# Kernel optimization log

Measured on AMD Instinct MI355X. Metric: run time of the kernel, lower is better.

Reference implementation:

```python
import jax, jax.numpy as jnp
import numpy as np

D_MODEL, D_STATE, EXPAND = 256, 16, 2
D_INNER = EXPAND * D_MODEL
DT_RANK = (D_MODEL + 15) // 16
BATCH, SEQLEN = 4, 4096


def silu(x):
    return x * jax.nn.sigmoid(x)


def setup_inputs() -> dict:
    key = jax.random.key(0)
    ks = jax.random.split(key, 10)
    h = jax.random.normal(ks[0], (BATCH, SEQLEN, D_MODEL), dtype=jnp.float32)
    Wi_f = jax.random.normal(ks[1], (2 * D_INNER, D_MODEL), dtype=jnp.float32) / np.sqrt(D_MODEL)
    Wi_b = jax.random.normal(ks[2], (2 * D_INNER, D_MODEL), dtype=jnp.float32) / np.sqrt(D_MODEL)
    Wx_f = jax.random.normal(ks[3], (DT_RANK + 2 * D_STATE, D_INNER), dtype=jnp.float32) / np.sqrt(D_INNER)
    Wx_b = jax.random.normal(ks[4], (DT_RANK + 2 * D_STATE, D_INNER), dtype=jnp.float32) / np.sqrt(D_INNER)
    dt_std = DT_RANK ** -0.5
    Wdt_f = jax.random.uniform(ks[5], (D_INNER, DT_RANK), dtype=jnp.float32, minval=-dt_std, maxval=dt_std)
    Wdt_b = jax.random.uniform(ks[6], (D_INNER, DT_RANK), dtype=jnp.float32, minval=-dt_std, maxval=dt_std)
    # dt bias = inverse-softplus of dt sampled log-uniform in [1e-3, 1e-1]
    dt = jnp.exp(jax.random.uniform(ks[7], (D_INNER,), dtype=jnp.float32) * (np.log(0.1) - np.log(0.001)) + np.log(0.001))
    dt = jnp.clip(dt, 1e-4, None)
    inv_dt = dt + jnp.log(-jnp.expm1(-dt))
    bdt_f = inv_dt
    bdt_b = inv_dt
    A_log = jnp.log(jnp.broadcast_to(jnp.arange(1, D_STATE + 1, dtype=jnp.float32), (D_INNER, D_STATE)))
    A_log_f = A_log
    A_log_b = A_log
    D_f = jnp.ones((D_INNER,), dtype=jnp.float32)
    D_b = jnp.ones((D_INNER,), dtype=jnp.float32)
    Wo = jax.random.normal(ks[8], (D_MODEL, 2 * D_INNER), dtype=jnp.float32) / np.sqrt(2 * D_INNER)
    return {"hidden_states": h, "Wi_f": Wi_f, "Wi_b": Wi_b, "Wx_f": Wx_f, "Wx_b": Wx_b,
            "Wdt_f": Wdt_f, "Wdt_b": Wdt_b, "bdt_f": bdt_f, "bdt_b": bdt_b,
            "A_log_f": A_log_f, "A_log_b": A_log_b, "D_f": D_f, "D_b": D_b, "Wo": Wo}


def mamba_dir(h, Wi, Wx, Wdt, bdt, A_log, Dp, reverse):
    b, l, _ = h.shape
    di, r = Wdt.shape
    n = A_log.shape[1]
    xz = h @ Wi.T                      # [b,l,2*di]
    if reverse:
        xz = xz[:, ::-1]
    x, z = xz[..., :di], xz[..., di:]
    u = silu(x)                        # selective_scan input u
    x_dbl = u @ Wx.T                   # [b,l,r+2n]
    delta = jax.nn.softplus(x_dbl[..., :r] @ Wdt.T + bdt)   # [b,l,di]
    Bm = x_dbl[..., r:r + n]           # [b,l,n]
    Cm = x_dbl[..., r + n:r + 2 * n]   # [b,l,n]
    A = -jnp.exp(A_log)                # [di,n]

    def step(s, inp):
        u_t, d_t, B_t, C_t = inp       # [b,di],[b,di],[b,n],[b,n]
        dA = jnp.exp(d_t[..., None] * A)                         # [b,di,n]
        s = dA * s + (d_t * u_t)[..., None] * B_t[:, None, :]    # [b,di,n]
        y_t = jnp.einsum('bdn,bn->bd', s, C_t)
        return s, y_t

    s0 = jnp.zeros((b, di, n), dtype=u.dtype)
    xs = (jnp.swapaxes(u, 0, 1), jnp.swapaxes(delta, 0, 1),
          jnp.swapaxes(Bm, 0, 1), jnp.swapaxes(Cm, 0, 1))
    _, ys = jax.lax.scan(step, s0, xs)
    y = jnp.swapaxes(ys, 0, 1) + u * Dp          # skip term D*u
    y = y * silu(z)                              # gated output
    if reverse:
        y = y[:, ::-1]
    return y


def reference(hidden_states, Wi_f, Wi_b, Wx_f, Wx_b, Wdt_f, Wdt_b, bdt_f, bdt_b, A_log_f, A_log_b, D_f, D_b, Wo):
    y_f = mamba_dir(hidden_states, Wi_f, Wx_f, Wdt_f, bdt_f, A_log_f, D_f, False)
    y_b = mamba_dir(hidden_states, Wi_b, Wx_b, Wdt_b, bdt_b, A_log_b, D_b, True)
    y = jnp.concatenate([y_f, y_b], axis=-1)     # [b,l,2*di]
    return y @ Wo.T                              # [b,l,d_model]
```

## Files before the change

### kernel.cpp

```cpp
#include <hip/hip_runtime.h>
#include <hip/hip_bf16.h>
#include <cstddef>
#include <cstdint>

#define D_MODELc 256
#define D_STATEc 16
#define D_INNERc 512
#define DT_RANKc 16
#define BATCHc   4
#define SEQLENc  4096
#define NCHUNK   128
#define CHUNK    32

typedef unsigned short u16;
typedef __attribute__((ext_vector_type(8))) short bf16x8;
typedef __attribute__((ext_vector_type(4))) float f32x4;
typedef float __attribute__((ext_vector_type(4))) f4v;

__device__ __forceinline__ float siluf(float v) { return v / (1.f + __expf(-v)); }

__device__ __forceinline__ u16 bf16_rne(float f) {
    uint32_t u = __float_as_uint(f);
    u += 0x7fffu + ((u >> 16) & 1u);
    return (u16)(u >> 16);
}
__device__ __forceinline__ float bf16_to_f(u16 h) {
    return __uint_as_float(((uint32_t)h) << 16);
}
__device__ __forceinline__ uint32_t pack_hl(float f) {
    u16 hh = bf16_rne(f);
    u16 ll = bf16_rne(f - bf16_to_f(hh));
    return ((uint32_t)hh << 16) | ll;
}
__device__ __forceinline__ float unpack_add(uint32_t v) {
    return __uint_as_float(v & 0xFFFF0000u) + __uint_as_float(v << 16);
}
__device__ __forceinline__ void unpack_frag(const uint32_t* q, bf16x8& fh, bf16x8& fl) {
    union { bf16x8 v; uint32_t w[4]; } H, L;
    #pragma unroll
    for (int i = 0; i < 4; i++) {
        uint32_t a = q[2 * i], b = q[2 * i + 1];
        H.w[i] = (a >> 16) | (b & 0xFFFF0000u);
        L.w[i] = (a & 0xFFFFu) | (b << 16);
    }
    fh = H.v; fl = L.v;
}
__device__ __forceinline__ float softplusf(float x) {
    return fmaxf(x, 0.f) + __logf(1.f + __expf(-fabsf(x)));
}
__device__ __forceinline__ float dot16_tree(const f4v x[4], const float* w, float bias) {
    float t0 = fmaf(x[0][1], w[1],  x[0][0] * w[0]);
    float t1 = fmaf(x[0][3], w[3],  x[0][2] * w[2]);
    float t2 = fmaf(x[1][1], w[5],  x[1][0] * w[4]);
    float t3 = fmaf(x[1][3], w[7],  x[1][2] * w[6]);
    float t4 = fmaf(x[2][1], w[9],  x[2][0] * w[8]);
    float t5 = fmaf(x[2][3], w[11], x[2][2] * w[10]);
    float t6 = fmaf(x[3][1], w[13], x[3][0] * w[12]);
    float t7 = fmaf(x[3][3], w[15], x[3][2] * w[14]);
    return bias + (((t0 + t1) + (t2 + t3)) + ((t4 + t5) + (t6 + t7)));
}
__device__ __forceinline__ void qladder(float q, float* qd) {
    float q2 = q * q;
    float q4 = q2 * q2;
    float q8 = q4 * q4;
    qd[0] = q;        qd[1] = q2;       qd[2] = q2 * q;     qd[3] = q4;
    qd[4] = q4 * q;   qd[5] = q4 * q2;  qd[6] = q4 * qd[2]; qd[7] = q8;
    qd[8] = q8 * q;   qd[9] = q8 * q2;  qd[10] = q8 * qd[2]; qd[11] = q8 * q4;
    qd[12] = q8 * qd[4]; qd[13] = q8 * qd[5]; qd[14] = q8 * qd[6]; qd[15] = q8 * q8;
}

#define GLL16(g, l) __builtin_amdgcn_global_load_lds( \
    (const __attribute__((address_space(1))) uint32_t*)(g), \
    (__attribute__((address_space(3))) uint32_t*)(l), 16, 0, 0)

__global__ __launch_bounds__(256) void split5_kernel(
        const float* __restrict__ s0, const float* __restrict__ s1,
        const float* __restrict__ s2, const float* __restrict__ s3,
        const float* __restrict__ s4,
        u16* __restrict__ h0, u16* __restrict__ l0,
        u16* __restrict__ h1, u16* __restrict__ l1,
        u16* __restrict__ h2, u16* __restrict__ l2,
        u16* __restrict__ h3, u16* __restrict__ l3,
        u16* __restrict__ h4, u16* __restrict__ l4,
        int n4w, int n4x) {
    const int which = blockIdx.y;
    const float* in; u16* hi; u16* lo; int n4;
    if      (which == 0) { in = s0; hi = h0; lo = l0; n4 = n4w; }
    else if (which == 1) { in = s1; hi = h1; lo = l1; n4 = n4w; }
    else if (which == 2) { in = s2; hi = h2; lo = l2; n4 = n4w; }
    else if (which == 3) { in = s3; hi = h3; lo = l3; n4 = n4x; }
    else                 { in = s4; hi = h4; lo = l4; n4 = n4x; }
    for (int i = blockIdx.x * 256 + threadIdx.x; i < n4; i += gridDim.x * 256) {
        float4 v = ((const float4*)in)[i];
        u16 a0 = bf16_rne(v.x), a1 = bf16_rne(v.y), a2 = bf16_rne(v.z), a3 = bf16_rne(v.w);
        ushort4 hv; hv.x = a0; hv.y = a1; hv.z = a2; hv.w = a3;
        ushort4 lv;
        lv.x = bf16_rne(v.x - bf16_to_f(a0));
        lv.y = bf16_rne(v.y - bf16_to_f(a1));
        lv.z = bf16_rne(v.z - bf16_to_f(a2));
        lv.w = bf16_rne(v.w - bf16_to_f(a3));
        ((ushort4*)hi)[i] = hv;
        ((ushort4*)lo)[i] = lv;
    }
}

__global__ __launch_bounds__(256) void split_kernel(const float* __restrict__ in,
                                                    u16* __restrict__ hi,
                                                    u16* __restrict__ lo, int n4) {
    int i = blockIdx.x * 256 + threadIdx.x;
    const int stride = gridDim.x * 256;
    for (; i < n4; i += stride) {
        float4 v = ((const float4*)in)[i];
        u16 a0 = bf16_rne(v.x), a1 = bf16_rne(v.y), a2 = bf16_rne(v.z), a3 = bf16_rne(v.w);
        ushort4 hv; hv.x = a0; hv.y = a1; hv.z = a2; hv.w = a3;
        ushort4 lv;
        lv.x = bf16_rne(v.x - bf16_to_f(a0));
        lv.y = bf16_rne(v.y - bf16_to_f(a1));
        lv.z = bf16_rne(v.z - bf16_to_f(a2));
        lv.w = bf16_rne(v.w - bf16_to_f(a3));
        ((ushort4*)hi)[i] = hv;
        ((ushort4*)lo)[i] = lv;
    }
}

template<int EPI, int NBL2, int AINT>
__global__ __launch_bounds__(256) void gemm_mfma(
        const u16* __restrict__ Ah, const u16* __restrict__ Al, int lda,
        const u16* __restrict__ Bh, const u16* __restrict__ Bl, int ldb,
        float* __restrict__ out0,
        uint32_t* __restrict__ uhl,
        int M, int N, int K) {
    __shared__ char lds[2][32768];
    const int t    = threadIdx.x;
    const int lane = t & 63;
    const int wid  = t >> 6;
    const int wrow = wid >> 1, wcol = wid & 1;

    const int id  = blockIdx.x;
    const int xcd = id & 7;
    const int j   = id >> 3;
    const int nb  = j & ((1 << NBL2) - 1);
    const int mg  = j >> NBL2;
    const int m0  = (mg * 8 + xcd) * 128;
    const int n0  = nb * 128;

    const int lr  = lane & 15;
    const int kgl = lane >> 4;

    f32x4 acc[4][4] = {};

    const char* gp[8];
    if (AINT == 0) {
        #pragma unroll
        for (int i = 0; i < 8; i++) {
            int c    = i * 256 + t;
            int tile = c >> 9;
            int kg   = (c >> 7) & 3;
            int row  = c & 127;
            const u16* bsrc = (tile == 0) ? Ah : (tile == 1) ? Al : (tile == 2) ? Bh : Bl;
            int r0 = (tile < 2) ? m0 : n0;
            int ld = (tile < 2) ? lda : ldb;
            gp[i] = (const char*)(bsrc + (size_t)(r0 + row) * ld + kg * 8);
        }
    } else {
        #pragma unroll
        for (int i = 0; i < 4; i++) {
            int c    = i * 256 + t;
            int kg   = c >> 8;
            int row  = (c >> 1) & 127;
            int half = c & 1;
            gp[i] = (const char*)((const uint32_t*)Ah + (size_t)(m0 + row) * lda + kg * 8 + half * 4);
        }
        #pragma unroll
        for (int i = 4; i < 8; i++) {
            int cb   = (i - 4) * 256 + t;
            int tile = cb >> 9;
            int kg   = (cb >> 7) & 3;
            int row  = cb & 127;
            const u16* bsrc = tile ? Bl : Bh;
            gp[i] = (const char*)(bsrc + (size_t)(n0 + row) * ldb + kg * 8);
        }
    }
    const int ldst_t = t << 4;

    auto stage = [&](int buf) {
        #pragma unroll
        for (int i = 0; i < 8; i++) {
            GLL16(gp[i], ((char*)lds) + buf * 32768 + i * 4096 + ldst_t);
            gp[i] += (AINT == 1 && i < 4) ? 128 : 64;
        }
    };

    const int NT = K >> 5;
    stage(0);
    __syncthreads();

    for (int kt = 0; kt < NT; ++kt) {
        const int buf = kt & 1;
        if (kt + 1 < NT) stage(buf ^ 1);

        bf16x8 afh[4], afl[4];
        if (AINT == 0) {
            const u16* lb = (const u16*)lds[buf];
            #pragma unroll
            for (int mi = 0; mi < 4; mi++) {
                int row = wrow * 64 + mi * 16 + lr;
                afh[mi] = *(const bf16x8*)(lb + 0 * 4096 + kgl * 1024 + row * 8);
                afl[mi] = *(const bf16x8*)(lb + 1 * 4096 + kgl * 1024 + row * 8);
            }
        } else {
            const uint32_t* la = (const uint32_t*)lds[buf];
            #pragma unroll
            for (int mi = 0; mi < 4; mi++) {
                int row = wrow * 64 + mi * 16 + lr;
                unpack_frag(la + kgl * 1024 + row * 8, afh[mi], afl[mi]);
            }
        }
        const u16* lbB = (const u16*)(lds[buf] + 16384);
        #pragma unroll
        for (int ni = 0; ni < 4; ni++) {
            int row = wcol * 64 + ni * 16 + lr;
            bf16x8 bfh = *(const bf16x8*)(lbB + 0 * 4096 + kgl * 1024 + row * 8);
            bf16x8 bfl = *(const bf16x8*)(lbB + 1 * 4096 + kgl * 1024 + row * 8);
            #pragma unroll
            for (int mi = 0; mi < 4; mi++) {
                acc[mi][ni] = __builtin_amdgcn_mfma_f32_16x16x32_bf16(afh[mi], bfh, acc[mi][ni], 0, 0, 0);
                acc[mi][ni] = __builtin_amdgcn_mfma_f32_16x16x32_bf16(afh[mi], bfl, acc[mi][ni], 0, 0, 0);
                acc[mi][ni] = __builtin_amdgcn_mfma_f32_16x16x32_bf16(afl[mi], bfh, acc[mi][ni], 0, 0, 0);
            }
        }
        __syncthreads();
    }

    #pragma unroll
    for (int mi = 0; mi < 4; mi++) {
        #pragma unroll
        for (int ni = 0; ni < 4; ni++) {
            #pragma unroll
            for (int r = 0; r < 4; r++) {
                int m = m0 + wrow * 64 + mi * 16 + kgl * 4 + r;
                int n = n0 + wcol * 64 + ni * 16 + lr;
                float v = acc[mi][ni][r];
                if (EPI == 0) {
                    __builtin_nontemporal_store(v, &out0[(size_t)m * N + n]);
                } else {
                    float s = siluf(v);
                    int dirn = n >> 10;
                    int nn   = n & 1023;
                    size_t dof = (size_t)dirn * (size_t)M * 512;
                    if (nn < 512) {
                        uhl[dof + (size_t)m * 512 + nn] = pack_hl(s);
                    } else {
                        out0[dof + (size_t)m * 512 + (nn - 512)] = s;
                    }
                }
            }
        }
    }
}

__global__ __launch_bounds__(256) void xdbl_mfma(
        const uint32_t* __restrict__ Uhl,
        const u16* __restrict__ WxH, const u16* __restrict__ WxL,
        float* __restrict__ out) {
    __shared__ uint32_t lds[4][64][8];
    const int t    = threadIdx.x;
    const int lane = t & 63;
    const int wid  = t >> 6;
    const int m0   = blockIdx.x * 64;
    const int dir  = blockIdx.y;
    const int Mp   = gridDim.x * 64;
    const int lr   = lane & 15;
    const int kgl  = lane >> 4;

    const size_t dofU = (size_t)dir * (size_t)Mp * 512;
    const size_t dofW = (size_t)dir * (size_t)48 * 512;

    const char* gp[2];
    #pragma unroll
    for (int i = 0; i < 2; i++) {
        int c    = i * 256 + t;
        int kg   = c >> 7;
        int row  = (c >> 1) & 63;
        int half = c & 1;
        gp[i] = (const char*)(Uhl + dofU + (size_t)(m0 + row) * 512 + kg * 8 + half * 4);
    }
    const int ldst_t = t << 4;

    f32x4 acc[3] = {};

    for (int k0 = 0; k0 < 512; k0 += 32) {
        #pragma unroll
        for (int i = 0; i < 2; i++) {
            GLL16(gp[i], ((char*)lds) + i * 4096 + ldst_t);
            gp[i] += 128;
        }
        __syncthreads();

        bf16x8 afh, afl;
        unpack_frag(&lds[kgl][wid * 16 + lr][0], afh, afl);
        #pragma unroll
        for (int nf = 0; nf < 3; nf++) {
            const size_t boff = dofW + (size_t)(nf * 16 + lr) * 512 + k0 + kgl * 8;
            bf16x8 bfh = *(const bf16x8*)(WxH + boff);
            bf16x8 bfl = *(const bf16x8*)(WxL + boff);
            acc[nf] = __builtin_amdgcn_mfma_f32_16x16x32_bf16(afh, bfh, acc[nf], 0, 0, 0);
            acc[nf] = __builtin_amdgcn_mfma_f32_16x16x32_bf16(afh, bfl, acc[nf], 0, 0, 0);
            acc[nf] = __builtin_amdgcn_mfma_f32_16x16x32_bf16(afl, bfh, acc[nf], 0, 0, 0);
        }
        __syncthreads();
    }

    float* o = out + (size_t)dir * (size_t)Mp * 48;
    #pragma unroll
    for (int nf = 0; nf < 3; nf++) {
        #pragma unroll
        for (int r = 0; r < 4; r++) {
            int m = m0 + wid * 16 + kgl * 4 + r;
            int n = nf * 16 + lr;
            o[(size_t)m * 48 + n] = acc[nf][r];
        }
    }
}

__global__ __launch_bounds__(256) void scan_phaseA(
        const uint32_t* __restrict__ Uhl,
        const float* __restrict__ XD,
        const float* __restrict__ Wdt_f, const float* __restrict__ Wdt_b,
        const float* __restrict__ bdt_f, const float* __restrict__ bdt_b,
        const float* __restrict__ AL_f, const float* __restrict__ AL_b,
        float* __restrict__ SDL, float* __restrict__ S) {
    const int c   = blockIdx.x;
    const int d   = blockIdx.y * 256 + threadIdx.x;
    const int z   = blockIdx.z;
    const int dir = z & 1;
    const int b   = z >> 1;
    const int PB  = gridDim.z >> 1;
    const int Mp  = PB * SEQLENc;
    const float* Wdt = dir ? Wdt_b : Wdt_f;
    const float* bdt = dir ? bdt_b : bdt_f;
    const float* AL  = dir ? AL_b  : AL_f;
    const uint32_t* UD = Uhl + (size_t)dir * Mp * 512;
    const float* XDD = XD + (size_t)dir * Mp * 48;

    float w[16], a[16], s[16];
    #pragma unroll
    for (int n = 0; n < 16; n++) {
        w[n] = Wdt[d * 16 + n];
        a[n] = -__expf(AL[d * 16 + n]);
        s[n] = 0.f;
    }
    const float a0 = a[0];
    bool pw = (a0 != 0.f);
    #pragma unroll
    for (int n = 1; n < 16; n++)
        pw = pw && (fabsf(a[n] - (float)(n + 1) * a0) <= 3e-6f * fabsf(a[n]));
    const float bb = bdt[d];
    float sdl = 0.f;

    for (int i = 0; i < CHUNK; i++) {
        int tt = c * CHUNK + i;
        int l  = dir ? (SEQLENc - 1 - tt) : tt;
        size_t row = (size_t)b * SEQLENc + l;
        float uu = unpack_add(UD[row * 512 + d]);
        const f4v* xr4 = (const f4v*)&XDD[row * 48];
        f4v xw[4] = {xr4[0], xr4[1], xr4[2], xr4[3]};
        float dl = softplusf(dot16_tree(xw, w, bb));
        sdl += dl;
        float du = dl * uu;
        if (pw) {
            float qd[16];
            qladder(__expf(a0 * dl), qd);
            #pragma unroll
            for (int g = 0; g < 4; g++) {
                f4v B4 = xr4[4 + g];
                #pragma unroll
                for (int jj = 0; jj < 4; jj++) {
                    int n = g * 4 + jj;
                    s[n] = fmaf(qd[n], s[n], du * B4[jj]);
                }
            }
        } else {
            #pragma unroll
            for (int g = 0; g < 4; g++) {
                f4v B4 = xr4[4 + g];
                #pragma unroll
                for (int jj = 0; jj < 4; jj++) {
                    int n = g * 4 + jj;
                    float dA = __expf(dl * a[n]);
                    s[n] = fmaf(dA, s[n], du * B4[jj]);
                }
            }
        }
    }
    SDL[((size_t)z * NCHUNK + c) * 512 + d] = sdl;
    size_t base = (((size_t)z * NCHUNK + c) * 16) * 512 + d;
    #pragma unroll
    for (int n = 0; n < 16; n++)
        S[base + (size_t)n * 512] = s[n];
}

__global__ __launch_bounds__(256) void scan_phaseB(const float* __restrict__ SDL,
                                                   float* __restrict__ S,
                                                   const float* __restrict__ AL_f,
                                                   const float* __restrict__ AL_b) {
    const int g   = blockIdx.x * 256 + threadIdx.x;
    const int d   = g & 511;
    const int n   = (g >> 9) & 15;
    const int z   = g >> 13;
    const int dir = z & 1;
    const float an = -__expf((dir ? AL_b : AL_f)[d * 16 + n]);
    const size_t strideS = (size_t)16 * 512;
    size_t offS = (((size_t)z * NCHUNK) * 16 + n) * 512 + d;
    size_t offD = ((size_t)z * NCHUNK) * 512 + d;
    float carry = 0.f;
    float sdl = SDL[offD], ss = S[offS];
    for (int c = 0; c < NCHUNK; c++) {
        float sdn = 0.f, sn = 0.f;
        if (c + 1 < NCHUNK) { sdn = SDL[offD + 512]; sn = S[offS + strideS]; }
        float pp = __expf(an * sdl);
        S[offS] = carry;
        carry = pp * carry + ss;
        sdl = sdn; ss = sn;
        offS += strideS; offD += 512;
    }
}

__global__ __launch_bounds__(256) void scan_phaseC(
        const uint32_t* __restrict__ Uhl,
        const float* __restrict__ XD,
        const float* __restrict__ Wdt_f, const float* __restrict__ Wdt_b,
        const float* __restrict__ bdt_f, const float* __restrict__ bdt_b,
        const float* __restrict__ AL_f, const float* __restrict__ AL_b,
        const float* __restrict__ E,
        const float* __restrict__ SZ,
        const float* __restrict__ D_f,  const float* __restrict__ D_b,
        uint32_t* __restrict__ Yhl) {
    const int c   = blockIdx.x;
    const int d   = blockIdx.y * 256 + threadIdx.x;
    const int z   = blockIdx.z;
    const int dir = z & 1;
    const int b   = z >> 1;
    const int PB  = gridDim.z >> 1;
    const int Mp  = PB * SEQLENc;
    const float* Wdt = dir ? Wdt_b : Wdt_f;
    const float* bdt = dir ? bdt_b : bdt_f;
    const float* AL  = dir ? AL_b  : AL_f;
    const uint32_t* UD = Uhl + (size_t)dir * Mp * 512;
    const float* XDD = XD + (size_t)dir * Mp * 48;
    const float* SZD = SZ + (size_t)dir * Mp * 512;

    float w[16], a[16], s[16];
    size_t base = (((size_t)z * NCHUNK + c) * 16) * 512 + d;
    #pragma unroll
    for (int n = 0; n < 16; n++) {
        w[n] = Wdt[d * 16 + n];
        a[n] = -__expf(AL[d * 16 + n]);
        s[n] = E[base + (size_t)n * 512];
    }
    const float a0 = a[0];
    bool pw = (a0 != 0.f);
    #pragma unroll
    for (int n = 1; n < 16; n++)
        pw = pw && (fabsf(a[n] - (float)(n + 1) * a0) <= 3e-6f * fabsf(a[n]));
    const float bb = bdt[d];
    const float Dd = (dir ? D_b : D_f)[d];

    for (int i = 0; i < CHUNK; i++) {
        int tt = c * CHUNK + i;
        int l  = dir ? (SEQLENc - 1 - tt) : tt;
        size_t row = (size_t)b * SEQLENc + l;
        float uu = unpack_add(UD[row * 512 + d]);
        const f4v* xr4 = (const f4v*)&XDD[row * 48];
        f4v xw[4] = {xr4[0], xr4[1], xr4[2], xr4[3]};
        float dl = softplusf(dot16_tree(xw, w, bb));
        float du = dl * uu;
        float yp0 = 0.f, yp1 = 0.f, yp2 = 0.f, yp3 = 0.f;
        if (pw) {
            float qd[16];
            qladder(__expf(a0 * dl), qd);
            #pragma unroll
            for (int g = 0; g < 4; g++) {
                f4v B4 = xr4[4 + g];
                f4v C4 = xr4[8 + g];
                float yp = 0.f;
                #pragma unroll
                for (int jj = 0; jj < 4; jj++) {
                    int n = g * 4 + jj;
                    s[n] = fmaf(qd[n], s[n], du * B4[jj]);
                    yp = fmaf(s[n], C4[jj], yp);
                }
                if (g == 0) yp0 = yp; else if (g == 1) yp1 = yp;
                else if (g == 2) yp2 = yp; else yp3 = yp;
            }
        } else {
            #pragma unroll
            for (int g = 0; g < 4; g++) {
                f4v B4 = xr4[4 + g];
                f4v C4 = xr4[8 + g];
                float yp = 0.f;
                #pragma unroll
                for (int jj = 0; jj < 4; jj++) {
                    int n = g * 4 + jj;
                    float dA = __expf(dl * a[n]);
                    s[n] = fmaf(dA, s[n], du * B4[jj]);
                    yp = fmaf(s[n], C4[jj], yp);
                }
                if (g == 0) yp0 = yp; else if (g == 1) yp1 = yp;
                else if (g == 2) yp2 = yp; else yp3 = yp;
            }
        }
        float y = (yp0 + yp1) + (yp2 + yp3);
        float sz = SZD[row * 512 + d];
        float yv = (y + uu * Dd) * sz;
        Yhl[row * 1024 + (size_t)dir * 512 + d] = pack_hl(yv);
    }
}

extern "C" void kernel_launch(void* const* d_in, const int* in_sizes, int n_in,
                              void* d_out, int out_size, void* d_ws, size_t ws_size,
                              hipStream_t stream) {
    const float* h    = (const float*)d_in[0];
    const float* Wi_f = (const float*)d_in[1];
    const float* Wi_b = (const float*)d_in[2];
    const float* Wx_f = (const float*)d_in[3];
    const float* Wx_b = (const float*)d_in[4];
    const float* Wdt_f= (const float*)d_in[5];
    const float* Wdt_b= (const float*)d_in[6];
    const float* bdt_f= (const float*)d_in[7];
    const float* bdt_b= (const float*)d_in[8];
    const float* Al_f = (const float*)d_in[9];
    const float* Al_b = (const float*)d_in[10];
    const float* D_f  = (const float*)d_in[11];
    const float* D_b  = (const float*)d_in[12];
    const float* Wo   = (const float*)d_in[13];
    float* out = (float*)d_out;

    const size_t W_ELE  = 1024 * 256;
    const size_t WX_ELE = 48 * 512;
    const size_t FB   = (size_t)SEQLENc * D_INNERc;
    const size_t FH   = (size_t)SEQLENc * D_MODELc;
    const size_t FX   = (size_t)SEQLENc * 48;
    const size_t FP   = (size_t)NCHUNK * 16 * 512;
    const size_t FD   = (size_t)NCHUNK * 512;
    const size_t FY   = (size_t)SEQLENc * 1024;

    const size_t fixed_bytes = (8 * W_ELE + 4 * WX_ELE) * sizeof(u16);
    const size_t per_b = 2 * FH * sizeof(u16)
                       + 2 * FB * sizeof(float)
                       + 2 * FB * sizeof(uint32_t)
                       + 2 * FX * sizeof(float)
                       + 2 * (FP + FD) * sizeof(float)
                       + FY * sizeof(uint32_t);
    int PB = 4;
    if (fixed_bytes + 4 * per_b + 65536 > ws_size) PB = 2;
    if (fixed_bytes + 2 * per_b + 65536 > ws_size) PB = 1;

    char* cur = (char*)d_ws;
    auto alloc = [&](size_t bytes) -> char* {
        char* p = cur; cur += (bytes + 255) & ~(size_t)255; return p;
    };
    u16* WiH = (u16*)alloc(2 * W_ELE * 2);
    u16* WiL = (u16*)alloc(2 * W_ELE * 2);
    u16* WoH = (u16*)alloc(W_ELE * 2);
    u16* WoL = (u16*)alloc(W_ELE * 2);
    u16* WxH = (u16*)alloc(2 * WX_ELE * 2);
    u16* WxL = (u16*)alloc(2 * WX_ELE * 2);
    u16*      hH  = (u16*)alloc((size_t)PB * FH * 2);
    u16*      hL  = (u16*)alloc((size_t)PB * FH * 2);
    float*    sz  = (float*)alloc((size_t)PB * 2 * FB * 4);
    uint32_t* uhl = (uint32_t*)alloc((size_t)PB * 2 * FB * 4);
    float*    xd  = (float*)alloc((size_t)PB * 2 * FX * 4);
    float*    SDL = (float*)alloc((size_t)PB * 2 * FD * 4);
    float*    S   = (float*)alloc((size_t)PB * 2 * FP * 4);
    uint32_t* yhl = (uint32_t*)alloc((size_t)PB * FY * 4);

    {
        int n4w = (int)(W_ELE / 4);
        int n4x = (int)(WX_ELE / 4);
        split5_kernel<<<dim3(64, 5), 256, 0, stream>>>(
            Wi_f, Wi_b, Wo, Wx_f, Wx_b,
            WiH, WiL, WiH + W_ELE, WiL + W_ELE, WoH, WoL,
            WxH, WxL, WxH + WX_ELE, WxL + WX_ELE,
            n4w, n4x);
    }

    for (int b0 = 0; b0 < BATCHc; b0 += PB) {
        const int Mp = PB * SEQLENc;
        const int MB = Mp / 128;
        const float* hB = h   + (size_t)b0 * FH;
        float*       oB = out + (size_t)b0 * FH;

        {
            int n4 = (int)((size_t)PB * FH / 4);
            int blocks = (n4 + 255) / 256; if (blocks > 2048) blocks = 2048;
            split_kernel<<<blocks, 256, 0, stream>>>(hB, hH, hL, n4);
        }

        gemm_mfma<1, 4, 0><<<16 * MB, 256, 0, stream>>>(
            hH, hL, D_MODELc, WiH, WiL, D_MODELc,
            sz, uhl, Mp, 2048, D_MODELc);

        xdbl_mfma<<<dim3(Mp / 64, 2), 256, 0, stream>>>(uhl, WxH, WxL, xd);

        scan_phaseA<<<dim3(NCHUNK, 2, 2 * PB), 256, 0, stream>>>(
            uhl, xd, Wdt_f, Wdt_b, bdt_f, bdt_b, Al_f, Al_b, SDL, S);
        scan_phaseB<<<PB * 64, 256, 0, stream>>>(SDL, S, Al_f, Al_b);
        scan_phaseC<<<dim3(NCHUNK, 2, 2 * PB), 256, 0, stream>>>(
            uhl, xd, Wdt_f, Wdt_b, bdt_f, bdt_b, Al_f, Al_b,
            S, sz, D_f, D_b, yhl);

        gemm_mfma<0, 1, 1><<<2 * MB, 256, 0, stream>>>(
            (const u16*)yhl, nullptr, 1024, WoH, WoL, 1024,
            oB, nullptr, Mp, D_MODELc, 1024);
    }
}
```

Before: 346.1 us.

## Deepen GEMM prefetch to two stages with vmcnt waits and alias Y onto SZ

The bf16x3 MFMA GEMM now issues global-to-LDS loads two tiles ahead. It waits with explicit s_waitcnt vmcnt counts and raw s_barrier instead of __syncthreads, so loads overlap more compute. Separately, the silu(z) buffer is laid out interleaved by direction [m][dir*512], and the scan output Yhl is written in place over it. This removes a separate Y workspace allocation, which can let larger batch partitions fit. The restrict qualifiers are dropped because the two buffers now alias, and the hand-counted vmcnt relies on the exact number of outstanding loads per stage.

```diff
diff --git a/kernel.cpp b/kernel.cpp
--- a/kernel.cpp
+++ b/kernel.cpp
@@ -16,6 +16,9 @@
 typedef __attribute__((ext_vector_type(8))) short bf16x8;
 typedef __attribute__((ext_vector_type(4))) float f32x4;
 typedef float __attribute__((ext_vector_type(4))) f4v;
+
+#define VMCNT8() asm volatile("s_waitcnt vmcnt(8)" ::: "memory")
+#define VMCNT0() asm volatile("s_waitcnt vmcnt(0)" ::: "memory")
 
 __device__ __forceinline__ float siluf(float v) { return v / (1.f + __expf(-v)); }
 
@@ -193,11 +196,14 @@
 
     const int NT = K >> 5;
     stage(0);
-    __syncthreads();
+    if (NT > 1) stage(1);
 
     for (int kt = 0; kt < NT; ++kt) {
         const int buf = kt & 1;
-        if (kt + 1 < NT) stage(buf ^ 1);
+        if (kt + 1 < NT) { VMCNT8(); } else { VMCNT0(); }
+        __builtin_amdgcn_sched_barrier(0);
+        __builtin_amdgcn_s_barrier();
+        __builtin_amdgcn_sched_barrier(0);
 
         bf16x8 afh[4], afl[4];
         if (AINT == 0) {
@@ -229,7 +235,10 @@
                 acc[mi][ni] = __builtin_amdgcn_mfma_f32_16x16x32_bf16(afl[mi], bfh, acc[mi][ni], 0, 0, 0);
             }
         }
-        __syncthreads();
+        __builtin_amdgcn_sched_barrier(0);
+        __builtin_amdgcn_s_barrier();
+        __builtin_amdgcn_sched_barrier(0);
+        if (kt + 2 < NT) stage(buf);
     }
 
     #pragma unroll
@@ -247,11 +256,11 @@
                     float s = siluf(v);
                     int dirn = n >> 10;
                     int nn   = n & 1023;
-                    size_t dof = (size_t)dirn * (size_t)M * 512;
                     if (nn < 512) {
+                        size_t dof = (size_t)dirn * (size_t)M * 512;
                         uhl[dof + (size_t)m * 512 + nn] = pack_hl(s);
                     } else {
-                        out0[dof + (size_t)m * 512 + (nn - 512)] = s;
+                        out0[(size_t)m * 1024 + dirn * 512 + (nn - 512)] = s;
                     }
                 }
             }
@@ -433,9 +442,9 @@
         const float* __restrict__ bdt_f, const float* __restrict__ bdt_b,
         const float* __restrict__ AL_f, const float* __restrict__ AL_b,
         const float* __restrict__ E,
-        const float* __restrict__ SZ,
+        const float* SZ,
         const float* __restrict__ D_f,  const float* __restrict__ D_b,
-        uint32_t* __restrict__ Yhl) {
+        uint32_t* Yhl) {
     const int c   = blockIdx.x;
     const int d   = blockIdx.y * 256 + threadIdx.x;
     const int z   = blockIdx.z;
@@ -448,7 +457,6 @@
     const float* AL  = dir ? AL_b  : AL_f;
     const uint32_t* UD = Uhl + (size_t)dir * Mp * 512;
     const float* XDD = XD + (size_t)dir * Mp * 48;
-    const float* SZD = SZ + (size_t)dir * Mp * 512;
 
     float w[16], a[16], s[16];
     size_t base = (((size_t)z * NCHUNK + c) * 16) * 512 + d;
@@ -511,9 +519,10 @@
             }
         }
         float y = (yp0 + yp1) + (yp2 + yp3);
-        float sz = SZD[row * 512 + d];
+        size_t zi = row * 1024 + (size_t)dir * 512 + d;
+        float sz = SZ[zi];
         float yv = (y + uu * Dd) * sz;
-        Yhl[row * 1024 + (size_t)dir * 512 + d] = pack_hl(yv);
+        Yhl[zi] = pack_hl(yv);
     }
 }
 
@@ -543,15 +552,13 @@
     const size_t FX   = (size_t)SEQLENc * 48;
     const size_t FP   = (size_t)NCHUNK * 16 * 512;
     const size_t FD   = (size_t)NCHUNK * 512;
-    const size_t FY   = (size_t)SEQLENc * 1024;
 
     const size_t fixed_bytes = (8 * W_ELE + 4 * WX_ELE) * sizeof(u16);
     const size_t per_b = 2 * FH * sizeof(u16)
                        + 2 * FB * sizeof(float)
                        + 2 * FB * sizeof(uint32_t)
                        + 2 * FX * sizeof(float)
-                       + 2 * (FP + FD) * sizeof(float)
-                       + FY * sizeof(uint32_t);
+                       + 2 * (FP + FD) * sizeof(float);
     int PB = 4;
     if (fixed_bytes + 4 * per_b + 65536 > ws_size) PB = 2;
     if (fixed_bytes + 2 * per_b + 65536 > ws_size) PB = 1;
@@ -573,7 +580,7 @@
     float*    xd  = (float*)alloc((size_t)PB * 2 * FX * 4);
     float*    SDL = (float*)alloc((size_t)PB * 2 * FD * 4);
     float*    S   = (float*)alloc((size_t)PB * 2 * FP * 4);
-    uint32_t* yhl = (uint32_t*)alloc((size_t)PB * FY * 4);
+    uint32_t* yhl = (uint32_t*)sz;
 
     {
         int n4w = (int)(W_ELE / 4);
```

Result: faster. 326.8 us (-5.6%).
